# Kernel tuning notes

Hardware: AMD Instinct MI355X
Metric: run time of the kernel (lower is better)

Reference implementation:

```python
import jax, jax.numpy as jnp
import numpy as np

HEADS = 8
DIM_HEAD = 64
SCALE = DIM_HEAD ** -0.5


def setup_inputs() -> dict:
    key = jax.random.key(0)
    ks = jax.random.split(key, 6)
    b, n, t, d, cond_dim, hidden = 2, 8, 1024, 512, 512, HEADS * DIM_HEAD
    return {
        "x": jax.random.normal(ks[0], (b * n, t, d), dtype=jnp.float32),
        "label_emb_mm": jax.random.normal(ks[1], (b, n, cond_dim), dtype=jnp.float32),
        "Wqkv": jax.random.normal(ks[2], (d, 3 * hidden), dtype=jnp.float32) * (d ** -0.5),
        "Wk": jax.random.normal(ks[3], (cond_dim, hidden), dtype=jnp.float32) * (cond_dim ** -0.5),
        "Wv": jax.random.normal(ks[4], (cond_dim, hidden), dtype=jnp.float32) * (cond_dim ** -0.5),
        "Wout": jax.random.normal(ks[5], (hidden, d), dtype=jnp.float32) * (hidden ** -0.5),
        "b": 2,
    }


def reference(x, label_emb_mm, Wqkv, Wk, Wv, Wout, b):
    bn, t, d = x.shape
    n = bn // b
    h, dh = HEADS, DIM_HEAD
    xb = x.reshape(b, n, t, d)
    # fused QKV projection: (b, n, t, 3*h*dh)
    qkv = xb @ Wqkv
    q, k, v = jnp.split(qkv, 3, axis=-1)

    def to_heads(z):  # (b, n, t, h*dh) -> (b, n, h, t, dh)
        return z.reshape(b, n, t, h, dh).transpose(0, 1, 3, 2, 4)

    q, k, v = to_heads(q), to_heads(k), to_heads(v)
    # per-frame conditioning K/V: one extra token per frame
    ek = (label_emb_mm @ Wk).reshape(b, n, 1, h, dh).transpose(0, 1, 3, 2, 4)
    ev = (label_emb_mm @ Wv).reshape(b, n, 1, h, dh).transpose(0, 1, 3, 2, 4)
    k = jnp.concatenate([ek, k], axis=-2)  # (b, n, h, 1+t, dh)
    v = jnp.concatenate([ev, v], axis=-2)
    q = q * SCALE
    sim = jnp.einsum("bnhid,bnhjd->bnhij", q, k)
    attn = jax.nn.softmax(sim, axis=-1)
    out = jnp.einsum("bnhij,bnhjd->bnhid", attn, v)
    out = out.transpose(0, 1, 3, 2, 4).reshape(b, n, t, h * dh)
    out = out @ Wout
    return out.reshape(b * n, t, d)
```

## Files before the change

### kernel.cpp

```cpp
#include <hip/hip_runtime.h>
#include <stdint.h>

typedef unsigned short u16;
typedef __bf16 bf16x8 __attribute__((ext_vector_type(8)));
typedef float f32x4 __attribute__((ext_vector_type(4)));
typedef float f32x16 __attribute__((ext_vector_type(16)));

__device__ __forceinline__ u16 f2bf(float f) {
  uint32_t u = __builtin_bit_cast(uint32_t, f);
  u += 0x7FFFu + ((u >> 16) & 1u);
  return (u16)(u >> 16);
}
__device__ __forceinline__ float bf2f(u16 v) {
  return __builtin_bit_cast(float, ((uint32_t)v) << 16);
}

#if __has_builtin(__builtin_amdgcn_exp2f)
__device__ __forceinline__ float exp2_fast(float x) { return __builtin_amdgcn_exp2f(x); }
#else
__device__ __forceinline__ float exp2_fast(float x) { return exp2f(x); }
#endif

__device__ __forceinline__ void gload_lds16(const u16* g, u16* l) {
  __builtin_amdgcn_global_load_lds(
      (const __attribute__((address_space(1))) uint32_t*)g,
      (__attribute__((address_space(3))) uint32_t*)l, 16, 0, 0);
}

__device__ __forceinline__ uint32_t cvtpk(float lo, float hi) {
  uint32_t r;
  asm("v_cvt_pk_bf16_f32 %0, %1, %2" : "=v"(r) : "v"(lo), "v"(hi));
  return r;
}
__device__ __forceinline__ void plswap(uint32_t& a, uint32_t& b) {
  asm volatile("v_permlane32_swap_b32 %0, %1" : "+v"(a), "+v"(b));
}

__global__ __launch_bounds__(256) void prep_kernel(
    const float* __restrict__ x, const float* __restrict__ Wqkv,
    const float* __restrict__ Wout, const float* __restrict__ label,
    const float* __restrict__ Wk, const float* __restrict__ Wv,
    u16* __restrict__ xb, u16* __restrict__ WqkvT, u16* __restrict__ WoutT,
    u16* __restrict__ ek, u16* __restrict__ ev, float qscale) {
  const int b = blockIdx.x;
  if (b < 4096) {
    int i = (b * 256 + threadIdx.x) * 8;
    float4 a = *(const float4*)(x + i);
    float4 c = *(const float4*)(x + i + 4);
    union { u16 u[8]; uint4 v; } r;
    r.u[0] = f2bf(a.x); r.u[1] = f2bf(a.y); r.u[2] = f2bf(a.z); r.u[3] = f2bf(a.w);
    r.u[4] = f2bf(c.x); r.u[5] = f2bf(c.y); r.u[6] = f2bf(c.z); r.u[7] = f2bf(c.w);
    *(uint4*)(xb + i) = r.v;
  } else if (b < 7168) {
    int id = (b - 4096) * 256 + threadIdx.x;
    int k = id & 511, nn = id >> 9;
    float v = Wqkv[(size_t)k * 1536 + nn];
    if (nn < 512) v *= qscale;
    WqkvT[id] = f2bf(v);
  } else if (b < 8192) {
    int id = (b - 7168) * 256 + threadIdx.x;
    int k = id & 511, nn = id >> 9;
    WoutT[id] = f2bf(Wout[(size_t)k * 512 + nn]);
  } else {
    __shared__ float sdata[256];
    const int bb = b - 8192;
    const int chunk = bb & 7, row = (bb >> 3) & 15;
    const float* W = (bb & 128) ? Wv : Wk;
    u16* o = (bb & 128) ? ev : ek;
    const int tid = threadIdx.x;
    const int col = chunk * 64 + (tid & 63);
    const int ks = tid >> 6;
    const float* lr = label + row * 512 + ks * 128;
    const float* wp = W + (size_t)(ks * 128) * 512 + col;
    float acc = 0.f;
#pragma unroll 8
    for (int i = 0; i < 128; ++i)
      acc = fmaf(lr[i], wp[(size_t)i * 512], acc);
    sdata[tid] = acc;
    __syncthreads();
    if (tid < 64) {
      float t = sdata[tid] + sdata[tid + 64] + sdata[tid + 128] + sdata[tid + 192];
      o[row * 512 + chunk * 64 + tid] = f2bf(t);
    }
  }
}

template <int MODE>
__global__ __launch_bounds__(256, 2) void gemm_bt_kernel(
    const u16* __restrict__ A, const u16* __restrict__ B,
    u16* __restrict__ OQ, u16* __restrict__ OKb, u16* __restrict__ OVT,
    float* __restrict__ OF, int K, int N) {
  constexpr int BN = (MODE == 0) ? 192 : 128;
  constexpr int NA = (MODE == 0) ? 8 : 4;
  constexpr int NB = (MODE == 0) ? 3 : 4;
  constexpr int A_ISS = 4;
  constexpr int B_ISS = BN / 32;
  constexpr int NBY = (MODE == 0) ? 8 : 4;

  __shared__ __align__(16) u16 As[2][128 * 64];
  __shared__ __align__(16) u16 Bs[2][BN * 64];

  const int tid = threadIdx.x;
  const int w = tid >> 6, lane = tid & 63;
  const int l15 = lane & 15, lg = lane >> 4;

  const int q8 = gridDim.x >> 3;
  const int wg = (blockIdx.x & 7) * q8 + (blockIdx.x >> 3);
  const int bx = wg / NBY, by = wg % NBY;

  const int srow = lane >> 3;
  const int schunk = (lane & 7) ^ srow;
  const u16* Ag = A + (size_t)(bx * 128 + srow) * K + schunk * 8;
  const u16* Bg = B + (size_t)(by * BN + srow) * K + schunk * 8;

  int aoff[NA][2], boff[NB][2];
#pragma unroll
  for (int mi = 0; mi < NA; ++mi)
#pragma unroll
    for (int ks = 0; ks < 2; ++ks) {
      const int row = ((MODE == 0) ? 0 : (w >> 1) * 64) + mi * 16 + l15;
      aoff[mi][ks] = row * 64 + (((ks * 4 + lg) ^ (row & 7)) * 8);
    }
#pragma unroll
  for (int ni = 0; ni < NB; ++ni)
#pragma unroll
    for (int ks = 0; ks < 2; ++ks) {
      const int row = ((MODE == 0) ? w * 48 : (w & 1) * 64) + ni * 16 + l15;
      boff[ni][ks] = row * 64 + (((ks * 4 + lg) ^ (row & 7)) * 8);
    }

  f32x4 acc[NA][NB] = {};

  const int nt = K >> 6;
#define STAGE(buf, k0)                                                        \
  {                                                                           \
    _Pragma("unroll") for (int i = 0; i < A_ISS; ++i) {                       \
      const int j = i * 4 + w;                                                \
      gload_lds16(Ag + (k0) + (size_t)(j * 8) * K, &As[buf][(j * 8) * 64]);   \
    }                                                                         \
    _Pragma("unroll") for (int i = 0; i < B_ISS; ++i) {                       \
      const int j = i * 4 + w;                                                \
      gload_lds16(Bg + (k0) + (size_t)(j * 8) * K, &Bs[buf][(j * 8) * 64]);   \
    }                                                                         \
  }
#define COMPUTE(cb)                                                           \
  {                                                                           \
    const u16* Ab = &As[cb][0];                                               \
    const u16* Bb = &Bs[cb][0];                                               \
    _Pragma("unroll") for (int ks = 0; ks < 2; ++ks) {                        \
      bf16x8 a[NA], b[NB];                                                    \
      _Pragma("unroll") for (int mi = 0; mi < NA; ++mi)                       \
          a[mi] = *(const bf16x8*)&Ab[aoff[mi][ks]];                          \
      _Pragma("unroll") for (int ni = 0; ni < NB; ++ni)                       \
          b[ni] = *(const bf16x8*)&Bb[boff[ni][ks]];                          \
      __builtin_amdgcn_s_setprio(1);                                          \
      _Pragma("unroll") for (int mi = 0; mi < NA; ++mi)                       \
          _Pragma("unroll") for (int ni = 0; ni < NB; ++ni)                   \
              acc[mi][ni] = __builtin_amdgcn_mfma_f32_16x16x32_bf16(           \
                  a[mi], b[ni], acc[mi][ni], 0, 0, 0);                        \
      __builtin_amdgcn_s_setprio(0);                                          \
    }                                                                         \
  }

  STAGE(0, 0);
  STAGE(1, 64);

  for (int t = 0; t < nt - 1; ++t) {
    if constexpr (A_ISS + B_ISS == 10)
      asm volatile("s_waitcnt vmcnt(10)" ::: "memory");
    else
      asm volatile("s_waitcnt vmcnt(8)" ::: "memory");
    __builtin_amdgcn_s_barrier();
    __builtin_amdgcn_sched_barrier(0);
    COMPUTE(t & 1);
    if (t + 2 < nt) {
      __builtin_amdgcn_s_barrier();
      __builtin_amdgcn_sched_barrier(0);
      STAGE(t & 1, (t + 2) * 64);
    }
  }
  asm volatile("s_waitcnt vmcnt(0)" ::: "memory");
  __builtin_amdgcn_s_barrier();
  __builtin_amdgcn_sched_barrier(0);
  COMPUTE((nt - 1) & 1);
#undef STAGE
#undef COMPUTE

  if constexpr (MODE == 1) {
    const int row0 = bx * 128 + (w >> 1) * 64 + lg * 4;
#pragma unroll
    for (int mi = 0; mi < NA; ++mi)
#pragma unroll
      for (int ni = 0; ni < NB; ++ni) {
        int col = by * BN + (w & 1) * 64 + ni * 16 + l15;
#pragma unroll
        for (int r = 0; r < 4; ++r)
          OF[(size_t)(row0 + mi * 16 + r) * N + col] = acc[mi][ni][r];
      }
  } else {
    const int row0 = bx * 128 + lg * 4;
#pragma unroll
    for (int mi = 0; mi < NA; ++mi)
#pragma unroll
      for (int ni = 0; ni < NB; ++ni) {
        const int gcol = by * BN + w * 48 + ni * 16 + l15;
        const int sect = gcol >> 9;
        const int colL = gcol & 511;
        if (sect < 2) {
          u16* O = sect ? OKb : OQ;
#pragma unroll
          for (int r = 0; r < 4; ++r)
            O[(size_t)(row0 + mi * 16 + r) * 512 + colL] = f2bf(acc[mi][ni][r]);
        } else {
          int h = colL >> 6, dh = colL & 63;
          int rr = row0 + mi * 16;
          int bn = rr >> 10, t0 = rr & 1023;
          ushort4 pk;
          pk.x = f2bf(acc[mi][ni][0]);
          pk.y = f2bf(acc[mi][ni][1]);
          pk.z = f2bf(acc[mi][ni][2]);
          pk.w = f2bf(acc[mi][ni][3]);
          *(ushort4*)&OVT[(size_t)((bn * 8 + h) * 64 + dh) * 1024 + t0] = pk;
        }
      }
  }
}

__global__ __launch_bounds__(256, 2) void attn_kernel(
    const u16* __restrict__ Qb, const u16* __restrict__ Kb, const u16* __restrict__ VTb,
    const u16* __restrict__ ekb, const u16* __restrict__ evb, u16* __restrict__ Ob) {
  __shared__ __align__(16) u16 Kl[64 * 64];
  __shared__ __align__(16) u16 Vl[64 * 64];

  const int tid = threadIdx.x;
  const int w = tid >> 6, lane = tid & 63;
  const int l31 = lane & 31, hi = lane >> 5;
  const int lb = (blockIdx.x & 7) * 64 + (blockIdx.x >> 3);
  const int head = lb >> 2, qt = lb & 3;
  const int bn = head >> 3, h = head & 7;
  const int q0 = qt * 256 + w * 64;

  const int sr = tid >> 3, sj = tid & 7;
  const int sdst = (sj ^ (sr & 7)) * 8;
  const u16* KgA = Kb + (size_t)(bn * 1024 + sr) * 512 + h * 64 + sj * 8;
  const u16* VgA = VTb + (size_t)(head * 64 + sr) * 1024 + sj * 8;
  u16* KlD = &Kl[sr * 64 + sdst];
  u16* VlD = &Vl[sr * 64 + sdst];

  uint4 kp0, kp1, vp0, vp1;
  {
    kp0 = *(const uint4*)(KgA);
    kp1 = *(const uint4*)(KgA + (size_t)32 * 512);
    vp0 = *(const uint4*)(VgA);
    vp1 = *(const uint4*)(VgA + (size_t)32 * 1024);
  }

  bf16x8 qf[2][4];
#pragma unroll
  for (int qs = 0; qs < 2; ++qs)
#pragma unroll
    for (int c = 0; c < 4; ++c)
      qf[qs][c] = *(const bf16x8*)(Qb + (size_t)(bn * 1024 + q0 + qs * 32 + l31) * 512 +
                                   h * 64 + c * 16 + hi * 8);

  bf16x8 bones1;
  {
    union { u16 u[8]; bf16x8 v; } ob;
#pragma unroll
    for (int j = 0; j < 8; ++j) ob.u[j] = (u16)0x3F80;
    bones1 = ob.v;
  }

  f32x16 acc[2][2];
  f32x16 acc5[2];
  {
    float dot[2] = {0.f, 0.f};
#pragma unroll
    for (int c = 0; c < 4; ++c) {
      bf16x8 ekf = *(const bf16x8*)(ekb + bn * 512 + h * 64 + c * 16 + hi * 8);
#pragma unroll
      for (int qs = 0; qs < 2; ++qs)
#pragma unroll
        for (int j = 0; j < 8; ++j)
          dot[qs] += (float)qf[qs][c][j] * (float)ekf[j];
    }
    union { u16 u[8]; bf16x8 v; } pef[2], evf[2];
#pragma unroll
    for (int qs = 0; qs < 2; ++qs) {
      uint32_t a = __builtin_bit_cast(uint32_t, dot[qs]), b = a;
      plswap(a, b);
      float part = (lane < 32) ? __builtin_bit_cast(float, b) : __builtin_bit_cast(float, a);
      float pe = exp2_fast(dot[qs] + part);
#pragma unroll
      for (int j = 0; j < 8; ++j) pef[qs].u[j] = 0;
      if (hi == 0) pef[qs].u[0] = f2bf(pe);
    }
#pragma unroll
    for (int dt = 0; dt < 2; ++dt) {
#pragma unroll
      for (int j = 0; j < 8; ++j) evf[dt].u[j] = 0;
      if (hi == 0) evf[dt].u[0] = evb[bn * 512 + h * 64 + dt * 32 + l31];
    }
    f32x16 z = {};
#pragma unroll
    for (int qs = 0; qs < 2; ++qs) {
#pragma unroll
      for (int dt = 0; dt < 2; ++dt)
        acc[qs][dt] = __builtin_amdgcn_mfma_f32_32x32x16_bf16(pef[qs].v, evf[dt].v, z, 0, 0, 0);
      acc5[qs] = __builtin_amdgcn_mfma_f32_32x32x16_bf16(pef[qs].v, bones1, z, 0, 0, 0);
    }
  }

  for (int jt = 0; jt < 16; ++jt) {
    __syncthreads();
    *(uint4*)(KlD) = kp0;
    *(uint4*)(KlD + 32 * 64) = kp1;
    *(uint4*)(VlD) = vp0;
    *(uint4*)(VlD + 32 * 64) = vp1;
    __syncthreads();

    if (jt < 15) {
      const int j0 = (jt + 1) * 64;
      kp0 = *(const uint4*)(KgA + (size_t)j0 * 512);
      kp1 = *(const uint4*)(KgA + (size_t)(j0 + 32) * 512);
      vp0 = *(const uint4*)(VgA + j0);
      vp1 = *(const uint4*)(VgA + j0 + (size_t)32 * 1024);
    }

#pragma unroll
    for (int sub = 0; sub < 2; ++sub) {
      const int rk = sub * 32 + l31;
      bf16x8 kb[4];
#pragma unroll
      for (int c = 0; c < 4; ++c)
        kb[c] = *(const bf16x8*)&Kl[rk * 64 + (((c * 2 + hi) ^ (rk & 7)) * 8)];

      f32x16 s[2] = {};
#pragma unroll
      for (int qs = 0; qs < 2; ++qs)
#pragma unroll
        for (int c = 0; c < 4; ++c)
          s[qs] = __builtin_amdgcn_mfma_f32_32x32x16_bf16(kb[c], qf[qs][c], s[qs], 0, 0, 0);

      bf16x8 pa[2][2];
#pragma unroll
      for (int qs = 0; qs < 2; ++qs) {
        uint32_t wd[8];
#pragma unroll
        for (int i = 0; i < 8; ++i)
          wd[i] = cvtpk(exp2_fast(s[qs][2 * i]), exp2_fast(s[qs][2 * i + 1]));
        plswap(wd[0], wd[2]);
        plswap(wd[1], wd[3]);
        plswap(wd[4], wd[6]);
        plswap(wd[5], wd[7]);
        union { uint32_t w[4]; bf16x8 v; } f0, f1;
        f0.w[0] = wd[0]; f0.w[1] = wd[1]; f0.w[2] = wd[2]; f0.w[3] = wd[3];
        f1.w[0] = wd[4]; f1.w[1] = wd[5]; f1.w[2] = wd[6]; f1.w[3] = wd[7];
        pa[qs][0] = f0.v;
        pa[qs][1] = f1.v;
      }

#pragma unroll
      for (int dt = 0; dt < 2; ++dt) {
        const int rv = dt * 32 + l31;
#pragma unroll
        for (int ch = 0; ch < 2; ++ch) {
          bf16x8 vb = *(const bf16x8*)&Vl[rv * 64 + (((sub * 4 + ch * 2 + hi) ^ (rv & 7)) * 8)];
#pragma unroll
          for (int qs = 0; qs < 2; ++qs)
            acc[qs][dt] = __builtin_amdgcn_mfma_f32_32x32x16_bf16(pa[qs][ch], vb, acc[qs][dt], 0, 0, 0);
        }
      }
#pragma unroll
      for (int qs = 0; qs < 2; ++qs)
#pragma unroll
        for (int ch = 0; ch < 2; ++ch)
          acc5[qs] = __builtin_amdgcn_mfma_f32_32x32x16_bf16(pa[qs][ch], bones1, acc5[qs], 0, 0, 0);
    }
  }

#pragma unroll
  for (int qs = 0; qs < 2; ++qs)
#pragma unroll
    for (int r = 0; r < 16; ++r) {
      const float inv = 1.0f / acc5[qs][r];
      const int q = q0 + qs * 32 + (r & 3) + 8 * (r >> 2) + 4 * hi;
      u16* op = Ob + (size_t)(bn * 1024 + q) * 512 + h * 64 + l31;
      op[0] = f2bf(acc[qs][0][r] * inv);
      op[32] = f2bf(acc[qs][1][r] * inv);
    }
}

extern "C" void kernel_launch(void* const* d_in, const int* in_sizes, int n_in,
                              void* d_out, int out_size, void* d_ws, size_t ws_size,
                              hipStream_t stream) {
  (void)in_sizes; (void)n_in; (void)out_size; (void)ws_size;
  const float* x     = (const float*)d_in[0];
  const float* label = (const float*)d_in[1];
  const float* Wqkv  = (const float*)d_in[2];
  const float* Wk    = (const float*)d_in[3];
  const float* Wv    = (const float*)d_in[4];
  const float* Wout  = (const float*)d_in[5];
  float* out = (float*)d_out;

  char* ws = (char*)d_ws;
  u16* xb    = (u16*)(ws);
  u16* WqkvT = (u16*)(ws + 16777216);
  u16* WoutT = (u16*)(ws + 18350080);
  u16* ekb   = (u16*)(ws + 18874368);
  u16* evb   = (u16*)(ws + 18890752);
  u16* Qbuf  = (u16*)(ws + 18907136);
  u16* Kbuf  = (u16*)(ws + 35684352);
  u16* VTbuf = (u16*)(ws + 52461568);

  const float qscale = 0.125f * 1.4426950408889634f;

  prep_kernel<<<8448, 256, 0, stream>>>(x, Wqkv, Wout, label, Wk, Wv,
                                        xb, WqkvT, WoutT, ekb, evb, qscale);

  gemm_bt_kernel<0><<<1024, 256, 0, stream>>>(xb, WqkvT, Qbuf, Kbuf, VTbuf, nullptr, 512, 1536);

  attn_kernel<<<512, 256, 0, stream>>>(Qbuf, Kbuf, VTbuf, ekb, evb, xb);

  gemm_bt_kernel<1><<<512, 256, 0, stream>>>(xb, WoutT, nullptr, nullptr, nullptr, out, 512, 512);
}
```

Measured before the change: 116.7 us.

## Double-buffer K/V tiles with direct global-to-LDS async loads in attention

```diff
diff --git a/kernel.cpp b/kernel.cpp
--- a/kernel.cpp
+++ b/kernel.cpp
@@ -229,8 +229,8 @@
 __global__ __launch_bounds__(256, 2) void attn_kernel(
     const u16* __restrict__ Qb, const u16* __restrict__ Kb, const u16* __restrict__ VTb,
     const u16* __restrict__ ekb, const u16* __restrict__ evb, u16* __restrict__ Ob) {
-  __shared__ __align__(16) u16 Kl[64 * 64];
-  __shared__ __align__(16) u16 Vl[64 * 64];
+  __shared__ __align__(16) u16 Kl[2][64 * 64];
+  __shared__ __align__(16) u16 Vl[2][64 * 64];
 
   const int tid = threadIdx.x;
   const int w = tid >> 6, lane = tid & 63;
@@ -240,20 +240,20 @@
   const int bn = head >> 3, h = head & 7;
   const int q0 = qt * 256 + w * 64;
 
-  const int sr = tid >> 3, sj = tid & 7;
-  const int sdst = (sj ^ (sr & 7)) * 8;
-  const u16* KgA = Kb + (size_t)(bn * 1024 + sr) * 512 + h * 64 + sj * 8;
-  const u16* VgA = VTb + (size_t)(head * 64 + sr) * 1024 + sj * 8;
-  u16* KlD = &Kl[sr * 64 + sdst];
-  u16* VlD = &Vl[sr * 64 + sdst];
-
-  uint4 kp0, kp1, vp0, vp1;
-  {
-    kp0 = *(const uint4*)(KgA);
-    kp1 = *(const uint4*)(KgA + (size_t)32 * 512);
-    vp0 = *(const uint4*)(VgA);
-    vp1 = *(const uint4*)(VgA + (size_t)32 * 1024);
-  }
+  const int srow = lane >> 3;
+  const int scol = ((lane & 7) ^ srow) * 8;
+  const u16* Kg0 = Kb + (size_t)(bn * 1024 + w * 16 + srow) * 512 + h * 64 + scol;
+  const u16* Vg0 = VTb + (size_t)(head * 64 + w * 16 + srow) * 1024 + scol;
+
+#define STAGE(buf, j0)                                                      \
+  {                                                                         \
+    gload_lds16(Kg0 + (size_t)(j0) * 512, &Kl[buf][(w * 16) * 64]);         \
+    gload_lds16(Kg0 + (size_t)((j0) + 8) * 512, &Kl[buf][(w * 16 + 8) * 64]); \
+    gload_lds16(Vg0 + (j0), &Vl[buf][(w * 16) * 64]);                       \
+    gload_lds16(Vg0 + (j0) + (size_t)8 * 1024, &Vl[buf][(w * 16 + 8) * 64]); \
+  }
+
+  STAGE(0, 0);
 
   bf16x8 qf[2][4];
 #pragma unroll
@@ -311,21 +311,11 @@
     }
   }
 
+  __syncthreads();
+
   for (int jt = 0; jt < 16; ++jt) {
-    __syncthreads();
-    *(uint4*)(KlD) = kp0;
-    *(uint4*)(KlD + 32 * 64) = kp1;
-    *(uint4*)(VlD) = vp0;
-    *(uint4*)(VlD + 32 * 64) = vp1;
-    __syncthreads();
-
-    if (jt < 15) {
-      const int j0 = (jt + 1) * 64;
-      kp0 = *(const uint4*)(KgA + (size_t)j0 * 512);
-      kp1 = *(const uint4*)(KgA + (size_t)(j0 + 32) * 512);
-      vp0 = *(const uint4*)(VgA + j0);
-      vp1 = *(const uint4*)(VgA + j0 + (size_t)32 * 1024);
-    }
+    const int buf = jt & 1;
+    if (jt < 15) STAGE(buf ^ 1, (jt + 1) * 64);
 
 #pragma unroll
     for (int sub = 0; sub < 2; ++sub) {
@@ -333,7 +323,7 @@
       bf16x8 kb[4];
 #pragma unroll
       for (int c = 0; c < 4; ++c)
-        kb[c] = *(const bf16x8*)&Kl[rk * 64 + (((c * 2 + hi) ^ (rk & 7)) * 8)];
+        kb[c] = *(const bf16x8*)&Kl[buf][rk * 64 + (((c * 2 + hi) ^ (rk & 7)) * 8)];
 
       f32x16 s[2] = {};
 #pragma unroll
@@ -365,7 +355,7 @@
         const int rv = dt * 32 + l31;
 #pragma unroll
         for (int ch = 0; ch < 2; ++ch) {
-          bf16x8 vb = *(const bf16x8*)&Vl[rv * 64 + (((sub * 4 + ch * 2 + hi) ^ (rv & 7)) * 8)];
+          bf16x8 vb = *(const bf16x8*)&Vl[buf][rv * 64 + (((sub * 4 + ch * 2 + hi) ^ (rv & 7)) * 8)];
 #pragma unroll
           for (int qs = 0; qs < 2; ++qs)
             acc[qs][dt] = __builtin_amdgcn_mfma_f32_32x32x16_bf16(pa[qs][ch], vb, acc[qs][dt], 0, 0, 0);
@@ -377,7 +367,10 @@
         for (int ch = 0; ch < 2; ++ch)
           acc5[qs] = __builtin_amdgcn_mfma_f32_32x32x16_bf16(pa[qs][ch], bones1, acc5[qs], 0, 0, 0);
     }
-  }
+
+    __syncthreads();
+  }
+#undef STAGE
 
 #pragma unroll
   for (int qs = 0; qs < 2; ++qs)
```

New measurement: 117.1 us. About the same (+0.4%).
